# Performance work log

Hardware: AMD Instinct MI355X
Metric: run time of the kernel (lower is better)

Reference implementation:

```python
import jax, jax.numpy as jnp
import numpy as np

N_NODES = 100000
N_EDGES = 3200000
IN_FEAT = 256
OUT_FEAT = 128

def setup_inputs() -> dict:
    key = jax.random.key(0)
    k1, k2, k3, k4, k5 = jax.random.split(key, 5)
    feat = jax.random.normal(k1, (N_NODES, IN_FEAT), dtype=jnp.float32)
    edge_row = jnp.sort(jax.random.randint(k2, (N_EDGES,), 0, N_NODES, dtype=jnp.int32))
    edge_col = jax.random.randint(k3, (N_EDGES,), 0, N_NODES, dtype=jnp.int32)
    edge_val = jax.random.uniform(k4, (N_EDGES,), dtype=jnp.float32)
    # Xavier-uniform init like the torch module
    limit = float(np.sqrt(6.0 / (IN_FEAT + OUT_FEAT)))
    weight = jax.random.uniform(k5, (IN_FEAT, OUT_FEAT), dtype=jnp.float32, minval=-limit, maxval=limit)
    return {"feat": feat, "edge_row": edge_row, "edge_col": edge_col, "edge_val": edge_val, "weight": weight}

def reference(feat, edge_row, edge_col, edge_val, weight):
    # feat_embedding = feat @ W            [N, out_feat]
    feat_embedding = jnp.matmul(feat, weight)
    # x = spmm(adj, feat_embedding): out[i] = sum_{edges e: row[e]=i} val[e] * femb[col[e]]
    messages = edge_val[:, None] * feat_embedding[edge_col]  # [E, out_feat]
    x = jax.ops.segment_sum(messages, edge_row, num_segments=N_NODES)
    return (feat_embedding, x)
```

## Files before the change

### kernel.cpp

```cpp
#include <hip/hip_runtime.h>
#include <hip/hip_fp16.h>

#define IN_FEAT 256
#define OUT_FEAT 128

#define GTM 128
#define KC  32

__global__ __launch_bounds__(256, 2) void gemm_kernel(
    const float* __restrict__ A, const float* __restrict__ W,
    float* __restrict__ C, __half* __restrict__ Ch, int M, int writeHalf)
{
    __shared__ float sA[KC][GTM];
    __shared__ float sW[KC][OUT_FEAT];

    const int t    = threadIdx.x;
    const int row0 = blockIdx.x * GTM;
    const int tr   = t >> 4;
    const int tc   = t & 15;

    float acc[8][8];
    #pragma unroll
    for (int i = 0; i < 8; ++i)
        #pragma unroll
        for (int j = 0; j < 8; ++j) acc[i][j] = 0.f;

    const int ar = t >> 1;
    const int ak = (t & 1) * 16;

    for (int kc = 0; kc < IN_FEAT; kc += KC) {
        {
            int grow = row0 + ar;
            const float* Ap = &A[(size_t)(grow < M ? grow : (M - 1)) * IN_FEAT + kc + ak];
            float4 a0 = *(const float4*)(Ap + 0);
            float4 a1 = *(const float4*)(Ap + 4);
            float4 a2 = *(const float4*)(Ap + 8);
            float4 a3 = *(const float4*)(Ap + 12);
            sA[ak + 0][ar] = a0.x; sA[ak + 1][ar] = a0.y; sA[ak + 2][ar] = a0.z; sA[ak + 3][ar] = a0.w;
            sA[ak + 4][ar] = a1.x; sA[ak + 5][ar] = a1.y; sA[ak + 6][ar] = a1.z; sA[ak + 7][ar] = a1.w;
            sA[ak + 8][ar] = a2.x; sA[ak + 9][ar] = a2.y; sA[ak +10][ar] = a2.z; sA[ak +11][ar] = a2.w;
            sA[ak +12][ar] = a3.x; sA[ak +13][ar] = a3.y; sA[ak +14][ar] = a3.z; sA[ak +15][ar] = a3.w;
        }
        {
            const float4* Wp  = (const float4*)&W[(size_t)kc * OUT_FEAT];
            float4*       sWp = (float4*)&sW[0][0];
            #pragma unroll
            for (int i = 0; i < 4; ++i) sWp[t + 256 * i] = Wp[t + 256 * i];
        }
        __syncthreads();

        #pragma unroll 8
        for (int k = 0; k < KC; ++k) {
            float4 a0v = *(const float4*)&sA[k][4 * tr];
            float4 a1v = *(const float4*)&sA[k][64 + 4 * tr];
            float4 w0v = *(const float4*)&sW[k][4 * tc];
            float4 w1v = *(const float4*)&sW[k][64 + 4 * tc];
            float av[8] = {a0v.x, a0v.y, a0v.z, a0v.w, a1v.x, a1v.y, a1v.z, a1v.w};
            float wv[8] = {w0v.x, w0v.y, w0v.z, w0v.w, w1v.x, w1v.y, w1v.z, w1v.w};
            #pragma unroll
            for (int ri = 0; ri < 8; ++ri)
                #pragma unroll
                for (int ci = 0; ci < 8; ++ci)
                    acc[ri][ci] = fmaf(av[ri], wv[ci], acc[ri][ci]);
        }
        __syncthreads();
    }

    #pragma unroll
    for (int ri = 0; ri < 8; ++ri) {
        int r = row0 + (ri < 4 ? 4 * tr + ri : 64 + 4 * tr + (ri - 4));
        if (r < M) {
            float4 o0 = {acc[ri][0], acc[ri][1], acc[ri][2], acc[ri][3]};
            float4 o1 = {acc[ri][4], acc[ri][5], acc[ri][6], acc[ri][7]};
            *(float4*)&C[(size_t)r * OUT_FEAT + 4 * tc]      = o0;
            *(float4*)&C[(size_t)r * OUT_FEAT + 64 + 4 * tc] = o1;
            if (writeHalf) {
                __half2 h01 = __floats2half2_rn(o0.x, o0.y);
                __half2 h23 = __floats2half2_rn(o0.z, o0.w);
                __half2 h45 = __floats2half2_rn(o1.x, o1.y);
                __half2 h67 = __floats2half2_rn(o1.z, o1.w);
                *(__half2*)&Ch[(size_t)r * OUT_FEAT + 4 * tc]          = h01;
                *(__half2*)&Ch[(size_t)r * OUT_FEAT + 4 * tc + 2]      = h23;
                *(__half2*)&Ch[(size_t)r * OUT_FEAT + 64 + 4 * tc]     = h45;
                *(__half2*)&Ch[(size_t)r * OUT_FEAT + 64 + 4 * tc + 2] = h67;
            }
        }
    }
}

__global__ void zero_kernel(float4* __restrict__ p, int n4)
{
    int i      = blockIdx.x * blockDim.x + threadIdx.x;
    int stride = gridDim.x * blockDim.x;
    for (; i < n4; i += stride) p[i] = float4{0.f, 0.f, 0.f, 0.f};
}

#define EPB 512
#define EPW 128
#define PF  16

template<int USE_H>
__global__ __launch_bounds__(256) void spmm_kernel(
    const int*   __restrict__ erow, const int* __restrict__ ecol,
    const float* __restrict__ eval, const float* __restrict__ femb,
    const __half* __restrict__ fembh, float* __restrict__ x, int E)
{
    __shared__ int   s_row[EPB];
    __shared__ int   s_col[EPB];
    __shared__ float s_val[EPB];

    const int blockBase = blockIdx.x * EPB;

    #pragma unroll
    for (int i = 0; i < 2; ++i) {
        int li = threadIdx.x + i * 256;
        int e  = blockBase + li;
        if (e < E) {
            s_row[li] = __builtin_nontemporal_load(&erow[e]);
            s_col[li] = __builtin_nontemporal_load(&ecol[e]);
            s_val[li] = __builtin_nontemporal_load(&eval[e]);
        }
    }
    __syncthreads();

    const int wave = threadIdx.x >> 6;
    const int lane = threadIdx.x & 63;
    const int j    = lane * 2;

    const int w0 = wave * EPW;
    const int g0 = blockBase + w0;
    if (g0 >= E) return;
    const int n = min(EPW, E - g0);

    float2 acc = {0.f, 0.f};
    int cur = s_row[w0];

    if (n == EPW) {
        #pragma unroll 1
        for (int base = 0; base < EPW; base += PF) {
            __half2 h[PF];
            float2  f[PF];
            if constexpr (USE_H) {
                #pragma unroll
                for (int i = 0; i < PF; ++i) {
                    int c = s_col[w0 + base + i];
                    h[i] = *(const __half2*)&fembh[(size_t)c * OUT_FEAT + j];
                }
            } else {
                #pragma unroll
                for (int i = 0; i < PF; ++i) {
                    int c = s_col[w0 + base + i];
                    f[i] = *(const float2*)&femb[(size_t)c * OUT_FEAT + j];
                }
            }
            #pragma unroll
            for (int i = 0; i < PF; ++i) {
                int r = s_row[w0 + base + i];
                if (r != cur) {
                    atomicAdd(&x[(size_t)cur * OUT_FEAT + j],     acc.x);
                    atomicAdd(&x[(size_t)cur * OUT_FEAT + j + 1], acc.y);
                    acc.x = 0.f; acc.y = 0.f;
                    cur = r;
                }
                float v = s_val[w0 + base + i];
                float2 fv;
                if constexpr (USE_H) fv = __half22float2(h[i]); else fv = f[i];
                acc.x = fmaf(v, fv.x, acc.x);
                acc.y = fmaf(v, fv.y, acc.y);
            }
        }
    } else {
        for (int idx = 0; idx < n; ++idx) {
            int r = s_row[w0 + idx];
            if (r != cur) {
                atomicAdd(&x[(size_t)cur * OUT_FEAT + j],     acc.x);
                atomicAdd(&x[(size_t)cur * OUT_FEAT + j + 1], acc.y);
                acc.x = 0.f; acc.y = 0.f;
                cur = r;
            }
            int c = s_col[w0 + idx];
            float v = s_val[w0 + idx];
            float2 fv;
            if constexpr (USE_H) fv = __half22float2(*(const __half2*)&fembh[(size_t)c * OUT_FEAT + j]);
            else                 fv = *(const float2*)&femb[(size_t)c * OUT_FEAT + j];
            acc.x = fmaf(v, fv.x, acc.x);
            acc.y = fmaf(v, fv.y, acc.y);
        }
    }
    atomicAdd(&x[(size_t)cur * OUT_FEAT + j],     acc.x);
    atomicAdd(&x[(size_t)cur * OUT_FEAT + j + 1], acc.y);
}

extern "C" void kernel_launch(void* const* d_in, const int* in_sizes, int n_in,
                              void* d_out, int out_size, void* d_ws, size_t ws_size,
                              hipStream_t stream)
{
    const float* feat = (const float*)d_in[0];
    const int*   erow = (const int*)  d_in[1];
    const int*   ecol = (const int*)  d_in[2];
    const float* eval = (const float*)d_in[3];
    const float* W    = (const float*)d_in[4];

    const int M = in_sizes[0] / IN_FEAT;
    const int E = in_sizes[1];

    float*  femb  = (float*)d_out;
    float*  x     = femb + (size_t)M * OUT_FEAT;
    __half* fembh = (__half*)d_ws;

    const size_t needH = (size_t)M * OUT_FEAT * sizeof(__half);
    const int useH = (ws_size >= needH) ? 1 : 0;

    gemm_kernel<<<(M + GTM - 1) / GTM, 256, 0, stream>>>(feat, W, femb, fembh, M, useH);

    zero_kernel<<<2048, 256, 0, stream>>>((float4*)x, (M * OUT_FEAT) / 4);

    int nblk = (E + EPB - 1) / EPB;
    if (useH) spmm_kernel<1><<<nblk, 256, 0, stream>>>(erow, ecol, eval, femb, fembh, x, E);
    else      spmm_kernel<0><<<nblk, 256, 0, stream>>>(erow, ecol, eval, femb, fembh, x, E);
}
```

Before: 391.2 us.

## Replace FP32 SIMT GEMM with FP16 MFMA GEMM using swizzled LDS

The feature-projection GEMM now converts A and W tiles to fp16 in shared memory, using an XOR swizzle to avoid bank conflicts, and computes the product with 16x16x32 fp16 MFMA instructions at fp32 accumulation. The goal is to cut the GEMM's FP32 FMA cost by moving it onto the matrix cores. In exchange, precision of the fp32 output drops because inputs are rounded to fp16. The epilogue now writes scalar elements instead of float4 vectors, and the whole 64KB K-dimension is staged at once.

```diff
diff --git a/kernel.cpp b/kernel.cpp
--- a/kernel.cpp
+++ b/kernel.cpp
@@ -4,85 +4,95 @@
 #define IN_FEAT 256
 #define OUT_FEAT 128
 
-#define GTM 128
-#define KC  32
-
-__global__ __launch_bounds__(256, 2) void gemm_kernel(
+typedef _Float16 half8 __attribute__((ext_vector_type(8)));
+typedef float    f32x4 __attribute__((ext_vector_type(4)));
+
+#define GBM 128
+#define GT  512
+
+__global__ __launch_bounds__(GT, 1) void gemm_mfma_kernel(
     const float* __restrict__ A, const float* __restrict__ W,
     float* __restrict__ C, __half* __restrict__ Ch, int M, int writeHalf)
 {
-    __shared__ float sA[KC][GTM];
-    __shared__ float sW[KC][OUT_FEAT];
+    __shared__ _Float16 sA[GBM * IN_FEAT];
+    __shared__ _Float16 sW[OUT_FEAT * IN_FEAT];
 
     const int t    = threadIdx.x;
-    const int row0 = blockIdx.x * GTM;
-    const int tr   = t >> 4;
-    const int tc   = t & 15;
-
-    float acc[8][8];
-    #pragma unroll
-    for (int i = 0; i < 8; ++i)
-        #pragma unroll
-        for (int j = 0; j < 8; ++j) acc[i][j] = 0.f;
-
-    const int ar = t >> 1;
-    const int ak = (t & 1) * 16;
-
-    for (int kc = 0; kc < IN_FEAT; kc += KC) {
-        {
-            int grow = row0 + ar;
-            const float* Ap = &A[(size_t)(grow < M ? grow : (M - 1)) * IN_FEAT + kc + ak];
-            float4 a0 = *(const float4*)(Ap + 0);
-            float4 a1 = *(const float4*)(Ap + 4);
-            float4 a2 = *(const float4*)(Ap + 8);
-            float4 a3 = *(const float4*)(Ap + 12);
-            sA[ak + 0][ar] = a0.x; sA[ak + 1][ar] = a0.y; sA[ak + 2][ar] = a0.z; sA[ak + 3][ar] = a0.w;
-            sA[ak + 4][ar] = a1.x; sA[ak + 5][ar] = a1.y; sA[ak + 6][ar] = a1.z; sA[ak + 7][ar] = a1.w;
-            sA[ak + 8][ar] = a2.x; sA[ak + 9][ar] = a2.y; sA[ak +10][ar] = a2.z; sA[ak +11][ar] = a2.w;
-            sA[ak +12][ar] = a3.x; sA[ak +13][ar] = a3.y; sA[ak +14][ar] = a3.z; sA[ak +15][ar] = a3.w;
-        }
-        {
-            const float4* Wp  = (const float4*)&W[(size_t)kc * OUT_FEAT];
-            float4*       sWp = (float4*)&sW[0][0];
-            #pragma unroll
-            for (int i = 0; i < 4; ++i) sWp[t + 256 * i] = Wp[t + 256 * i];
-        }
-        __syncthreads();
-
-        #pragma unroll 8
-        for (int k = 0; k < KC; ++k) {
-            float4 a0v = *(const float4*)&sA[k][4 * tr];
-            float4 a1v = *(const float4*)&sA[k][64 + 4 * tr];
-            float4 w0v = *(const float4*)&sW[k][4 * tc];
-            float4 w1v = *(const float4*)&sW[k][64 + 4 * tc];
-            float av[8] = {a0v.x, a0v.y, a0v.z, a0v.w, a1v.x, a1v.y, a1v.z, a1v.w};
-            float wv[8] = {w0v.x, w0v.y, w0v.z, w0v.w, w1v.x, w1v.y, w1v.z, w1v.w};
-            #pragma unroll
-            for (int ri = 0; ri < 8; ++ri)
-                #pragma unroll
-                for (int ci = 0; ci < 8; ++ci)
-                    acc[ri][ci] = fmaf(av[ri], wv[ci], acc[ri][ci]);
-        }
-        __syncthreads();
-    }
-
-    #pragma unroll
-    for (int ri = 0; ri < 8; ++ri) {
-        int r = row0 + (ri < 4 ? 4 * tr + ri : 64 + 4 * tr + (ri - 4));
-        if (r < M) {
-            float4 o0 = {acc[ri][0], acc[ri][1], acc[ri][2], acc[ri][3]};
-            float4 o1 = {acc[ri][4], acc[ri][5], acc[ri][6], acc[ri][7]};
-            *(float4*)&C[(size_t)r * OUT_FEAT + 4 * tc]      = o0;
-            *(float4*)&C[(size_t)r * OUT_FEAT + 64 + 4 * tc] = o1;
-            if (writeHalf) {
-                __half2 h01 = __floats2half2_rn(o0.x, o0.y);
-                __half2 h23 = __floats2half2_rn(o0.z, o0.w);
-                __half2 h45 = __floats2half2_rn(o1.x, o1.y);
-                __half2 h67 = __floats2half2_rn(o1.z, o1.w);
-                *(__half2*)&Ch[(size_t)r * OUT_FEAT + 4 * tc]          = h01;
-                *(__half2*)&Ch[(size_t)r * OUT_FEAT + 4 * tc + 2]      = h23;
-                *(__half2*)&Ch[(size_t)r * OUT_FEAT + 64 + 4 * tc]     = h45;
-                *(__half2*)&Ch[(size_t)r * OUT_FEAT + 64 + 4 * tc + 2] = h67;
+    const int row0 = blockIdx.x * GBM;
+
+    {
+        const int row = t >> 2;
+        const int kq  = t & 3;
+        int grow = row0 + row; if (grow >= M) grow = M - 1;
+        const float* Ap = &A[(size_t)grow * IN_FEAT];
+        #pragma unroll
+        for (int i = 0; i < 8; ++i) {
+            int k = kq * 8 + i * 32;
+            float4 a0 = *(const float4*)(Ap + k);
+            float4 a1 = *(const float4*)(Ap + k + 4);
+            half8 h;
+            h[0]=(_Float16)a0.x; h[1]=(_Float16)a0.y; h[2]=(_Float16)a0.z; h[3]=(_Float16)a0.w;
+            h[4]=(_Float16)a1.x; h[5]=(_Float16)a1.y; h[6]=(_Float16)a1.z; h[7]=(_Float16)a1.w;
+            int byte = row * 512 + k * 2;
+            byte ^= (row & 7) << 4;
+            *(half8*)((char*)sA + byte) = h;
+        }
+    }
+    {
+        const int col = t & 127;
+        const int kq  = t >> 7;
+        #pragma unroll
+        for (int i = 0; i < 16; ++i) {
+            int k = kq * 64 + i * 4;
+            _Float16 h[4];
+            h[0] = (_Float16)W[(size_t)(k+0) * OUT_FEAT + col];
+            h[1] = (_Float16)W[(size_t)(k+1) * OUT_FEAT + col];
+            h[2] = (_Float16)W[(size_t)(k+2) * OUT_FEAT + col];
+            h[3] = (_Float16)W[(size_t)(k+3) * OUT_FEAT + col];
+            int byte = col * 512 + k * 2;
+            byte ^= (col & 7) << 4;
+            *(unsigned long long*)((char*)sW + byte) = *(const unsigned long long*)h;
+        }
+    }
+    __syncthreads();
+
+    const int wid  = t >> 6;
+    const int lane = t & 63;
+    const int rowBase = wid * 16;
+    const int fr = lane & 15;
+    const int fk = lane >> 4;
+
+    f32x4 acc[8];
+    #pragma unroll
+    for (int nt = 0; nt < 8; ++nt) acc[nt] = (f32x4){0.f, 0.f, 0.f, 0.f};
+
+    #pragma unroll
+    for (int ks = 0; ks < 8; ++ks) {
+        const int arow  = rowBase + fr;
+        int abyte = arow * 512 + ks * 64 + fk * 16;
+        abyte ^= (arow & 7) << 4;
+        half8 af = *(const half8*)((const char*)sA + abyte);
+        #pragma unroll
+        for (int nt = 0; nt < 8; ++nt) {
+            const int col = nt * 16 + fr;
+            int bbyte = col * 512 + ks * 64 + fk * 16;
+            bbyte ^= (col & 7) << 4;
+            half8 bf = *(const half8*)((const char*)sW + bbyte);
+            acc[nt] = __builtin_amdgcn_mfma_f32_16x16x32_f16(af, bf, acc[nt], 0, 0, 0);
+        }
+    }
+
+    const int drow = fk * 4;
+    #pragma unroll
+    for (int nt = 0; nt < 8; ++nt) {
+        #pragma unroll
+        for (int r = 0; r < 4; ++r) {
+            int grow = row0 + rowBase + drow + r;
+            if (grow < M) {
+                int col = nt * 16 + fr;
+                C[(size_t)grow * OUT_FEAT + col] = acc[nt][r];
+                if (writeHalf)
+                    *(_Float16*)&Ch[(size_t)grow * OUT_FEAT + col] = (_Float16)acc[nt][r];
             }
         }
     }
@@ -211,7 +221,7 @@
     const size_t needH = (size_t)M * OUT_FEAT * sizeof(__half);
     const int useH = (ws_size >= needH) ? 1 : 0;
 
-    gemm_kernel<<<(M + GTM - 1) / GTM, 256, 0, stream>>>(feat, W, femb, fembh, M, useH);
+    gemm_mfma_kernel<<<(M + GBM - 1) / GBM, GT, 0, stream>>>(feat, W, femb, fembh, M, useH);
 
     zero_kernel<<<2048, 256, 0, stream>>>((float4*)x, (M * OUT_FEAT) / 4);
 
```

Result: faster. 362.0 us (-7.5%).
